# Kernel optimization log

Hardware: AMD Instinct MI355X
Metric: run time of the kernel (lower is better)

The kernel has to match this reference:

```python
import jax, jax.numpy as jnp
import numpy as np
from jax import lax

B, DIM, H, W = 8, 256, 48, 48
HEADS, DH = 8, 32
K, S = 5, 2
P = K // 2
SCALE = DH ** -0.5
EPS = 1e-5


def setup_inputs() -> dict:
    key = jax.random.key(0)
    ks = jax.random.split(key, 12)
    w = lambda k, sh: jax.random.normal(k, sh, jnp.float32) * 0.02
    return {
        'x': jax.random.normal(ks[0], (B, DIM, H, W), jnp.float32),
        'kv': jax.random.normal(ks[1], (B, DIM, H, W), jnp.float32),
        'wq': w(ks[2], (DIM, DIM)), 'bq': jnp.zeros((DIM,), jnp.float32),
        'wk': w(ks[3], (DIM, DIM)), 'bk': jnp.zeros((DIM,), jnp.float32),
        'wv': w(ks[4], (DIM, DIM)), 'bv': jnp.zeros((DIM,), jnp.float32),
        'w_dw': w(ks[5], (DH, 1, K, K)), 'b_dw': jnp.zeros((DH,), jnp.float32),
        'ln_w': jnp.ones((DH,), jnp.float32), 'ln_b': jnp.zeros((DH,), jnp.float32),
        'w_off': w(ks[6], (2, DH)),
        'wo': w(ks[7], (DIM, DIM)), 'bo': jnp.zeros((DIM,), jnp.float32),
    }


def conv1x1(x, w, b=None):
    # x: (B, Cin, H, W), w: (Cout, Cin)
    y = jnp.einsum('oc,bchw->bohw', w, x)
    return y if b is None else y + b[None, :, None, None]


def grid_sample_bilinear(inp, grid):
    # inp: (N, C, Hh, Ww); grid: (N, Hg, Wg, 2) in (x, y), align_corners=True
    N, C, Hh, Ww = inp.shape
    gx = (grid[..., 0] + 1.0) * 0.5 * (Ww - 1)
    gy = (grid[..., 1] + 1.0) * 0.5 * (Hh - 1)
    x0 = jnp.floor(gx)
    y0 = jnp.floor(gy)
    wx = gx - x0  # frac weights for x1/y1 corners
    wy = gy - y0
    x0i = jnp.clip(x0.astype(jnp.int32), 0, Ww - 1)
    x1i = jnp.clip(x0.astype(jnp.int32) + 1, 0, Ww - 1)
    y0i = jnp.clip(y0.astype(jnp.int32), 0, Hh - 1)
    y1i = jnp.clip(y0.astype(jnp.int32) + 1, 0, Hh - 1)
    flat = inp.reshape(N, C, Hh * Ww)
    n = grid.shape[1] * grid.shape[2]

    def gather(yi, xi):
        idx = (yi * Ww + xi).reshape(N, 1, n)
        return jnp.take_along_axis(flat, jnp.broadcast_to(idx, (N, C, n)), axis=2)

    w00 = ((1 - wx) * (1 - wy)).reshape(N, 1, n)
    w01 = (wx * (1 - wy)).reshape(N, 1, n)
    w10 = ((1 - wx) * wy).reshape(N, 1, n)
    w11 = (wx * wy).reshape(N, 1, n)
    return (w00 * gather(y0i, x0i) + w01 * gather(y0i, x1i)
            + w10 * gather(y1i, x0i) + w11 * gather(y1i, x1i))  # (N, C, n)


def reference(x, kv, wq, bq, wk, bk, wv, bv, w_dw, b_dw, ln_w, ln_b, w_off, wo, bo):
    q = conv1x1(x, wq, bq)                      # (B, DIM, H, W)
    q_off = q.reshape(B * HEADS, DH, H, W)      # per-head channels
    # depthwise offset conv
    t = lax.conv_general_dilated(q_off, w_dw, (S, S), [(P, P), (P, P)],
                                 feature_group_count=DH,
                                 dimension_numbers=('NCHW', 'OIHW', 'NCHW'))
    t = t + b_dw[None, :, None, None]
    Hk, Wk = t.shape[2], t.shape[3]
    n = Hk * Wk
    # LayerNormProxy: LN over channel dim
    t = t.transpose(0, 2, 3, 1)                 # (BH, Hk, Wk, DH)
    mu = t.mean(-1, keepdims=True)
    var = ((t - mu) ** 2).mean(-1, keepdims=True)
    t = (t - mu) / jnp.sqrt(var + EPS) * ln_w + ln_b
    t = jax.nn.gelu(t, approximate=False)
    offset = jnp.einsum('oc,bhwc->bhwo', w_off, t)  # (BH, Hk, Wk, 2) as (y, x)
    # reference points, normalized to [-1, 1]
    ref_y = (jnp.linspace(0.5, Hk - 0.5, Hk, dtype=jnp.float32) / (Hk - 1.0)) * 2.0 - 1.0
    ref_x = (jnp.linspace(0.5, Wk - 0.5, Wk, dtype=jnp.float32) / (Wk - 1.0)) * 2.0 - 1.0
    ref = jnp.stack(jnp.meshgrid(ref_y, ref_x, indexing='ij'), axis=-1)  # (Hk, Wk, 2)
    pos = jnp.clip(offset + ref[None], -1.0, 1.0)
    grid = pos[..., ::-1]                       # (x, y) order for sampling
    kvs = grid_sample_bilinear(kv.reshape(B * HEADS, DH, H, W), grid)  # (BH, DH, n)
    kv4 = kvs.reshape(B, DIM, 1, n)
    k = conv1x1(kv4, wk, bk).reshape(B * HEADS, DH, n)
    v = conv1x1(kv4, wv, bv).reshape(B * HEADS, DH, n)
    qf = q.reshape(B * HEADS, DH, H * W)
    attn = jax.nn.softmax(jnp.einsum('bcm,bcn->bmn', qf, k) * SCALE, axis=2)
    out = jnp.einsum('bmn,bcn->bcm', attn, v).reshape(B, DIM, H, W)
    return conv1x1(out, wo, bo)
```

## Files before the change

### kernel.cpp

```cpp
#include <hip/hip_runtime.h>
#include <hip/hip_bf16.h>
#include <cstddef>

#define BB 8
#define DIM 256
#define HH 48
#define WW 48
#define HW 2304
#define HEADS 8
#define DH 32
#define BH 64
#define HK 24
#define WK 24
#define NN 576
#define SCALE 0.17677669529663687f
#define EPSF 1e-5f

typedef __attribute__((ext_vector_type(8))) short short8;
typedef __attribute__((ext_vector_type(4))) float f32x4;

static __device__ inline short f2bf_s(float f) {
  __hip_bfloat16 h = __float2bfloat16(f);
  return *reinterpret_cast<short*>(&h);
}

static __device__ inline unsigned pkrnd(float a, float b) {
  unsigned ua = __builtin_bit_cast(unsigned, a) + 0x8000u;
  unsigned ub = __builtin_bit_cast(unsigned, b) + 0x8000u;
  return __builtin_amdgcn_perm(ub, ua, 0x07060302);
}

static __device__ inline void split8(const float* xf, short8& bh, short8& bl) {
  union { unsigned u[4]; short8 v; } H, L;
#pragma unroll
  for (int p = 0; p < 4; p++) {
    float x0 = xf[2 * p], x1 = xf[2 * p + 1];
    unsigned u0 = __builtin_bit_cast(unsigned, x0) & 0xffff0000u;
    unsigned u1 = __builtin_bit_cast(unsigned, x1) & 0xffff0000u;
    float l0 = x0 - __builtin_bit_cast(float, u0);
    float l1 = x1 - __builtin_bit_cast(float, u1);
    H.u[p] = __builtin_amdgcn_perm(u1, u0, 0x07060302);
    L.u[p] = __builtin_amdgcn_perm(__builtin_bit_cast(unsigned, l1),
                                   __builtin_bit_cast(unsigned, l0), 0x07060302);
  }
  bh = H.v;
  bl = L.v;
}

__global__ __launch_bounds__(256) void prep(
    const float* __restrict__ x,
    const float* __restrict__ wq, const float* __restrict__ wk,
    const float* __restrict__ wv, const float* __restrict__ wo,
    short* __restrict__ Xh, short* __restrict__ Xl,
    short* __restrict__ Wqh, short* __restrict__ Wql,
    short* __restrict__ Wkh, short* __restrict__ Wkl,
    short* __restrict__ Wvh, short* __restrict__ Wvl,
    short* __restrict__ Woh, short* __restrict__ Wol) {
  const int bid = blockIdx.x;
  if (bid < 1152) {
    __shared__ float t[64][65];
    int mt = bid % 36, t2 = bid / 36;
    int ct = t2 & 3, b = t2 >> 2;
    const int c0 = ct * 64, m0 = mt * 64;
    const int col = threadIdx.x & 63, row4 = threadIdx.x >> 6;
    const float* xb = x + ((size_t)b * 256 + c0) * HW + m0;
#pragma unroll
    for (int k = 0; k < 16; k++) {
      int c = row4 + k * 4;
      t[c][col] = xb[(size_t)c * HW + col];
    }
    __syncthreads();
    short* oh = Xh + ((size_t)b * HW + m0) * 256 + c0;
    short* ol = Xl + ((size_t)b * HW + m0) * 256 + c0;
#pragma unroll
    for (int k = 0; k < 16; k++) {
      int m = row4 + k * 4;
      float v = t[col][m];
      unsigned u = __builtin_bit_cast(unsigned, v) & 0xffff0000u;
      float rem = v - __builtin_bit_cast(float, u);
      oh[(size_t)m * 256 + col] = (short)(u >> 16);
      ol[(size_t)m * 256 + col] = (short)(__builtin_bit_cast(unsigned, rem) >> 16);
    }
  } else {
    const float* srcs[4] = {wq, wk, wv, wo};
    short* his[4] = {Wqh, Wkh, Wvh, Woh};
    short* los[4] = {Wql, Wkl, Wvl, Wol};
    int e0 = (bid - 1152) * 1024 + threadIdx.x * 4;
    int w = e0 >> 16, off = e0 & 65535;
    float4 v4 = *(const float4*)(srcs[w] + off);
    float vv[4] = {v4.x, v4.y, v4.z, v4.w};
    union { short s[4]; int2 i2; } Hu, Lu;
#pragma unroll
    for (int j = 0; j < 4; j++) {
      unsigned u = __builtin_bit_cast(unsigned, vv[j]) & 0xffff0000u;
      float rem = vv[j] - __builtin_bit_cast(float, u);
      Hu.s[j] = (short)(u >> 16);
      Lu.s[j] = (short)(__builtin_bit_cast(unsigned, rem) >> 16);
    }
    *(int2*)(his[w] + off) = Hu.i2;
    *(int2*)(los[w] + off) = Lu.i2;
  }
}

__global__ __launch_bounds__(256) void gemm_q_mfma(const short* __restrict__ Wh,
                                                   const short* __restrict__ Wl,
                                                   const float* __restrict__ bias,
                                                   const short* __restrict__ Xh,
                                                   const short* __restrict__ Xl,
                                                   float* __restrict__ Y) {
  const int tid = threadIdx.x;
  const int wave = tid >> 6;
  const int lane = tid & 63;
  const int quad = lane >> 4, l15 = lane & 15;
  const int b = blockIdx.y;
  const int oBase = wave * 64;
  const int mBase = blockIdx.x * 64;

  f32x4 acc[4][4] = {};
  for (int kc = 0; kc < 256; kc += 32) {
    short8 ah[4], al[4];
#pragma unroll
    for (int os = 0; os < 4; os++) {
      ah[os] = *(const short8*)(Wh + (size_t)(oBase + os * 16 + l15) * 256 + kc + quad * 8);
      al[os] = *(const short8*)(Wl + (size_t)(oBase + os * 16 + l15) * 256 + kc + quad * 8);
    }
#pragma unroll
    for (int mt = 0; mt < 4; mt++) {
      short8 bh_ = *(const short8*)(Xh + ((size_t)b * HW + mBase + mt * 16 + l15) * 256 + kc + quad * 8);
      short8 bl_ = *(const short8*)(Xl + ((size_t)b * HW + mBase + mt * 16 + l15) * 256 + kc + quad * 8);
#pragma unroll
      for (int os = 0; os < 4; os++) {
        acc[os][mt] = __builtin_amdgcn_mfma_f32_16x16x32_bf16(ah[os], bh_, acc[os][mt], 0, 0, 0);
        acc[os][mt] = __builtin_amdgcn_mfma_f32_16x16x32_bf16(al[os], bh_, acc[os][mt], 0, 0, 0);
        acc[os][mt] = __builtin_amdgcn_mfma_f32_16x16x32_bf16(ah[os], bl_, acc[os][mt], 0, 0, 0);
      }
    }
  }

#pragma unroll
  for (int os = 0; os < 4; os++)
#pragma unroll
    for (int r = 0; r < 4; r++) {
      int o = oBase + os * 16 + quad * 4 + r;
      float bs = bias[o];
      float* yp = Y + ((size_t)b * 256 + o) * HW + mBase + l15;
#pragma unroll
      for (int mt = 0; mt < 4; mt++) yp[mt * 16] = acc[os][mt][r] + bs;
    }
}

__global__ __launch_bounds__(64) void dw_sample_kernel(
    const float* __restrict__ q, const float* __restrict__ kv,
    const float* __restrict__ w_dw, const float* __restrict__ b_dw,
    const float* __restrict__ ln_w, const float* __restrict__ ln_b,
    const float* __restrict__ w_off, short* __restrict__ kvsTh,
    short* __restrict__ kvsTl) {
  __shared__ float s_wdw[DH * 25];
  __shared__ float s_bdw[DH], s_lnw[DH], s_lnb[DH], s_woff[2 * DH];
  const int tid = threadIdx.x;
  for (int i = tid; i < DH * 25; i += 64) s_wdw[i] = w_dw[i];
  if (tid < DH) { s_bdw[tid] = b_dw[tid]; s_lnw[tid] = ln_w[tid]; s_lnb[tid] = ln_b[tid]; }
  if (tid < 2 * DH) s_woff[tid] = w_off[tid];
  __syncthreads();

  const int nl = tid & 15, cg = tid >> 4;
  const int c0 = cg * 8;
  const int bh = blockIdx.x / (NN / 16);
  const int ntile = blockIdx.x - bh * (NN / 16);
  const int n = ntile * 16 + nl;
  const int yk = n / WK, xk = n - yk * WK;

  const float* qb = q + (size_t)bh * DH * HW;
  float t[8];
#pragma unroll
  for (int j = 0; j < 8; j++) t[j] = s_bdw[c0 + j];

  const int y0r = yk * 2 - 2, x0r = xk * 2 - 2;
  for (int dy = 0; dy < 5; dy++) {
    int y = y0r + dy;
    if (y < 0 || y >= HH) continue;
    for (int dx = 0; dx < 5; dx++) {
      int x = x0r + dx;
      if (x < 0 || x >= WW) continue;
      int off = y * WW + x;
      int widx = dy * 5 + dx;
#pragma unroll
      for (int j = 0; j < 8; j++)
        t[j] += s_wdw[(c0 + j) * 25 + widx] * qb[(size_t)(c0 + j) * HW + off];
    }
  }

  float mu = 0.f;
#pragma unroll
  for (int j = 0; j < 8; j++) mu += t[j];
  mu += __shfl_xor(mu, 16);
  mu += __shfl_xor(mu, 32);
  mu *= (1.0f / DH);
  float var = 0.f;
#pragma unroll
  for (int j = 0; j < 8; j++) { float d = t[j] - mu; var += d * d; }
  var += __shfl_xor(var, 16);
  var += __shfl_xor(var, 32);
  var *= (1.0f / DH);
  float rstd = rsqrtf(var + EPSF);

  float o0 = 0.f, o1 = 0.f;
#pragma unroll
  for (int j = 0; j < 8; j++) {
    float xn = (t[j] - mu) * rstd * s_lnw[c0 + j] + s_lnb[c0 + j];
    float g = 0.5f * xn * (1.0f + erff(xn * 0.70710678118654752f));
    o0 += s_woff[c0 + j] * g;
    o1 += s_woff[DH + c0 + j] * g;
  }
  o0 += __shfl_xor(o0, 16);
  o0 += __shfl_xor(o0, 32);
  o1 += __shfl_xor(o1, 16);
  o1 += __shfl_xor(o1, 32);

  const float ref_y = (0.5f + (float)yk) / 23.0f * 2.0f - 1.0f;
  const float ref_x = (0.5f + (float)xk) / 23.0f * 2.0f - 1.0f;
  float py = fminf(fmaxf(o0 + ref_y, -1.0f), 1.0f);
  float px = fminf(fmaxf(o1 + ref_x, -1.0f), 1.0f);

  float gx = (px + 1.0f) * 0.5f * 47.0f;
  float gy = (py + 1.0f) * 0.5f * 47.0f;
  float x0f = floorf(gx), y0f = floorf(gy);
  float wx = gx - x0f, wy = gy - y0f;
  int x0 = (int)x0f, y0 = (int)y0f;
  int x0i = min(max(x0, 0), WW - 1);
  int x1i = min(max(x0 + 1, 0), WW - 1);
  int y0i = min(max(y0, 0), HH - 1);
  int y1i = min(max(y0 + 1, 0), HH - 1);
  float w00 = (1.f - wx) * (1.f - wy);
  float w01 = wx * (1.f - wy);
  float w10 = (1.f - wx) * wy;
  float w11 = wx * wy;
  int i00 = y0i * WW + x0i, i01 = y0i * WW + x1i;
  int i10 = y1i * WW + x0i, i11 = y1i * WW + x1i;

  const float* kvb = kv + ((size_t)bh * DH + c0) * HW;
  float val[8];
#pragma unroll
  for (int j = 0; j < 8; j++) {
    const float* p = kvb + (size_t)j * HW;
    val[j] = w00 * p[i00] + w01 * p[i01] + w10 * p[i10] + w11 * p[i11];
  }
  short8 hv, lv;
  split8(val, hv, lv);
  size_t idx = ((size_t)(bh >> 3) * NN + n) * 256 + (bh & 7) * DH + c0;
  *(short8*)(kvsTh + idx) = hv;
  *(short8*)(kvsTl + idx) = lv;
}

__global__ __launch_bounds__(256) void kv_gemm_mfma(
    const short* __restrict__ Wkh, const short* __restrict__ Wkl,
    const float* __restrict__ bk,
    const short* __restrict__ Wvh, const short* __restrict__ Wvl,
    const float* __restrict__ bv,
    const short* __restrict__ Xh, const short* __restrict__ Xl,
    short* __restrict__ Kb, short* __restrict__ Vb) {
  const int tid = threadIdx.x;
  const int wave = tid >> 6;
  const int lane = tid & 63;
  const int quad = lane >> 4, l15 = lane & 15;
  const int b = blockIdx.z;
  const int mode = blockIdx.y >> 2;
  const int oTile = (blockIdx.y & 3) * 64;
  const int nBase = blockIdx.x * 64;

  if (mode == 0) {
    const int nW = nBase + wave * 16;
    const short* arh = Xh + ((size_t)b * NN + nW + l15) * 256 + quad * 8;
    const short* arl = Xl + ((size_t)b * NN + nW + l15) * 256 + quad * 8;
    f32x4 acc[4] = {};
    for (int kc = 0; kc < 256; kc += 32) {
      short8 ah = *(const short8*)(arh + kc);
      short8 al = *(const short8*)(arl + kc);
#pragma unroll
      for (int ot = 0; ot < 4; ot++) {
        short8 bh_ = *(const short8*)(Wkh + (size_t)(oTile + ot * 16 + l15) * 256 + kc + quad * 8);
        short8 bl_ = *(const short8*)(Wkl + (size_t)(oTile + ot * 16 + l15) * 256 + kc + quad * 8);
        acc[ot] = __builtin_amdgcn_mfma_f32_16x16x32_bf16(ah, bh_, acc[ot], 0, 0, 0);
        acc[ot] = __builtin_amdgcn_mfma_f32_16x16x32_bf16(al, bh_, acc[ot], 0, 0, 0);
        acc[ot] = __builtin_amdgcn_mfma_f32_16x16x32_bf16(ah, bl_, acc[ot], 0, 0, 0);
      }
    }
    float bs[4];
#pragma unroll
    for (int ot = 0; ot < 4; ot++) bs[ot] = bk[oTile + ot * 16 + l15];
#pragma unroll
    for (int r = 0; r < 4; r++) {
      short* yp = Kb + ((size_t)b * NN + nW + quad * 4 + r) * 256 + oTile + l15;
#pragma unroll
      for (int ot = 0; ot < 4; ot++) yp[ot * 16] = f2bf_s(acc[ot][r] + bs[ot]);
    }
  } else {
    const int oW = oTile + wave * 16;
    const short* arh = Wvh + (size_t)(oW + l15) * 256 + quad * 8;
    const short* arl = Wvl + (size_t)(oW + l15) * 256 + quad * 8;
    f32x4 acc[4] = {};
    for (int kc = 0; kc < 256; kc += 32) {
      short8 ah = *(const short8*)(arh + kc);
      short8 al = *(const short8*)(arl + kc);
#pragma unroll
      for (int nt = 0; nt < 4; nt++) {
        short8 bh_ = *(const short8*)(Xh + ((size_t)b * NN + nBase + nt * 16 + l15) * 256 + kc + quad * 8);
        short8 bl_ = *(const short8*)(Xl + ((size_t)b * NN + nBase + nt * 16 + l15) * 256 + kc + quad * 8);
        acc[nt] = __builtin_amdgcn_mfma_f32_16x16x32_bf16(ah, bh_, acc[nt], 0, 0, 0);
        acc[nt] = __builtin_amdgcn_mfma_f32_16x16x32_bf16(al, bh_, acc[nt], 0, 0, 0);
        acc[nt] = __builtin_amdgcn_mfma_f32_16x16x32_bf16(ah, bl_, acc[nt], 0, 0, 0);
      }
    }
#pragma unroll
    for (int r = 0; r < 4; r++) {
      int o = oW + quad * 4 + r;
      float bs = bv[o];
      short* yp = Vb + ((size_t)b * 256 + o) * NN + nBase + l15;
#pragma unroll
      for (int nt = 0; nt < 4; nt++) yp[nt * 16] = f2bf_s(acc[nt][r] + bs);
    }
  }
}

__global__ __launch_bounds__(256) void attn_mfma(const float* __restrict__ q,
                                                 const short* __restrict__ Kb,
                                                 const short* __restrict__ Vb,
                                                 short* __restrict__ O) {
  __shared__ short sK[2][64 * 40];
  __shared__ short sV[2][32 * 88];
  __shared__ int sP[4][2][256];
  const int tid = threadIdx.x;
  const int wave = tid >> 6;
  const int lane = tid & 63;
  const int quad = lane >> 4;
  const int l15 = lane & 15;
  const int bh = blockIdx.y;
  const int b = bh >> 3, head = bh & 7;
  const int mBase = blockIdx.x * 128 + wave * 32;

  short8 bq[2];
#pragma unroll
  for (int mt = 0; mt < 2; mt++) {
    const float* qp = q + ((size_t)bh * DH + quad * 8) * HW + mBase + mt * 16 + l15;
    short8 v;
#pragma unroll
    for (int j = 0; j < 8; j++) v[j] = f2bf_s(qp[(size_t)j * HW] * SCALE);
    bq[mt] = v;
  }

  const int kn = tid >> 2, kc = (tid & 3) * 8;
  const int vc = tid >> 3, vn = (tid & 7) * 8;
  const short* kg = Kb + (size_t)b * NN * 256 + head * DH;
  const short* vg = Vb + ((size_t)b * 256 + head * DH) * NN;

  short8 kreg = *(const short8*)(kg + (size_t)kn * 256 + kc);
  short8 vreg = *(const short8*)(vg + (size_t)vc * NN + vn);
  *(short8*)(&sK[0][kn * 40 + kc]) = kreg;
  *(short8*)(&sV[0][vc * 88 + vn]) = vreg;
  __syncthreads();

  const int g = (l15 >> 1) & 3;
  const int row16 = l15 * 16;
  const int wr0 = row16 + (((quad >> 1) ^ g) << 2) + ((quad & 1) << 1);
  const int wr1 = row16 + (((2 + (quad >> 1)) ^ g) << 2) + ((quad & 1) << 1);
  const int rd = row16 + ((quad ^ g) << 2);

  f32x4 oacc[2][2] = {};
  f32x4 dacc[2] = {};
  const short ONE = 0x3F80;
  const short8 ones = {ONE, ONE, ONE, ONE, ONE, ONE, ONE, ONE};

  for (int s = 0; s < 9; s++) {
    const int buf = s & 1;
    if (s + 1 < 9) {
      kreg = *(const short8*)(kg + (size_t)((s + 1) * 64 + kn) * 256 + kc);
      vreg = *(const short8*)(vg + (size_t)vc * NN + (s + 1) * 64 + vn);
    }
#pragma unroll
    for (int nt = 0; nt < 2; nt++) {
      short8 ka0 = *(const short8*)(&sK[buf][(nt * 32 + l15) * 40 + quad * 8]);
      short8 ka1 = *(const short8*)(&sK[buf][(nt * 32 + 16 + l15) * 40 + quad * 8]);
      short8 va0 = *(const short8*)(&sV[buf][l15 * 88 + nt * 32 + quad * 8]);
      short8 va1 = *(const short8*)(&sV[buf][(16 + l15) * 88 + nt * 32 + quad * 8]);
      f32x4 z = {0.f, 0.f, 0.f, 0.f};
      f32x4 st[2][2];
      st[0][0] = __builtin_amdgcn_mfma_f32_16x16x32_bf16(ka0, bq[0], z, 0, 0, 0);
      st[0][1] = __builtin_amdgcn_mfma_f32_16x16x32_bf16(ka1, bq[0], z, 0, 0, 0);
      st[1][0] = __builtin_amdgcn_mfma_f32_16x16x32_bf16(ka0, bq[1], z, 0, 0, 0);
      st[1][1] = __builtin_amdgcn_mfma_f32_16x16x32_bf16(ka1, bq[1], z, 0, 0, 0);
#pragma unroll
      for (int mt = 0; mt < 2; mt++) {
        float p0 = __expf(st[mt][0][0]), p1 = __expf(st[mt][0][1]);
        float p2 = __expf(st[mt][0][2]), p3 = __expf(st[mt][0][3]);
        float p4 = __expf(st[mt][1][0]), p5 = __expf(st[mt][1][1]);
        float p6 = __expf(st[mt][1][2]), p7 = __expf(st[mt][1][3]);
        int* base = &sP[wave][mt][0];
        *(int2*)(base + wr0) = make_int2((int)pkrnd(p0, p1), (int)pkrnd(p2, p3));
        *(int2*)(base + wr1) = make_int2((int)pkrnd(p4, p5), (int)pkrnd(p6, p7));
      }
#pragma unroll
      for (int mt = 0; mt < 2; mt++) {
        short8 pa = *(short8*)(&sP[wave][mt][0] + rd);
        oacc[mt][0] = __builtin_amdgcn_mfma_f32_16x16x32_bf16(pa, va0, oacc[mt][0], 0, 0, 0);
        oacc[mt][1] = __builtin_amdgcn_mfma_f32_16x16x32_bf16(pa, va1, oacc[mt][1], 0, 0, 0);
        dacc[mt] = __builtin_amdgcn_mfma_f32_16x16x32_bf16(pa, ones, dacc[mt], 0, 0, 0);
      }
    }
    if (s + 1 < 9) {
      *(short8*)(&sK[buf ^ 1][kn * 40 + kc]) = kreg;
      *(short8*)(&sV[buf ^ 1][vc * 88 + vn]) = vreg;
    }
    __syncthreads();
  }

#pragma unroll
  for (int mt = 0; mt < 2; mt++) {
    short* ob = O + ((size_t)b * HW + mBase + mt * 16) * 256 + head * DH + l15;
#pragma unroll
    for (int r = 0; r < 4; r++) {
      float inv = 1.0f / dacc[mt][r];
      ob[(size_t)(quad * 4 + r) * 256] = f2bf_s(oacc[mt][0][r] * inv);
      ob[(size_t)(quad * 4 + r) * 256 + 16] = f2bf_s(oacc[mt][1][r] * inv);
    }
  }
}

__global__ __launch_bounds__(256) void wo_gemm_mfma(const short* __restrict__ Whi,
                                                    const short* __restrict__ Wlo,
                                                    const float* __restrict__ bias,
                                                    const short* __restrict__ X,
                                                    float* __restrict__ Y) {
  const int tid = threadIdx.x;
  const int wave = tid >> 6;
  const int lane = tid & 63;
  const int quad = lane >> 4;
  const int l15 = lane & 15;
  const int b = blockIdx.y;
  const int oBase = wave * 64;
  const int mBase = blockIdx.x * 64;

  f32x4 acc[4][4] = {};
  for (int kc = 0; kc < 256; kc += 32) {
    short8 ah[4], al[4];
#pragma unroll
    for (int os = 0; os < 4; os++) {
      ah[os] = *(const short8*)(Whi + (size_t)(oBase + os * 16 + l15) * 256 + kc + quad * 8);
      al[os] = *(const short8*)(Wlo + (size_t)(oBase + os * 16 + l15) * 256 + kc + quad * 8);
    }
#pragma unroll
    for (int mt = 0; mt < 4; mt++) {
      short8 bx = *(const short8*)(X + ((size_t)b * HW + mBase + mt * 16 + l15) * 256 + kc + quad * 8);
#pragma unroll
      for (int os = 0; os < 4; os++) {
        acc[os][mt] = __builtin_amdgcn_mfma_f32_16x16x32_bf16(ah[os], bx, acc[os][mt], 0, 0, 0);
        acc[os][mt] = __builtin_amdgcn_mfma_f32_16x16x32_bf16(al[os], bx, acc[os][mt], 0, 0, 0);
      }
    }
  }

#pragma unroll
  for (int os = 0; os < 4; os++)
#pragma unroll
    for (int r = 0; r < 4; r++) {
      int o = oBase + os * 16 + quad * 4 + r;
      float bs = bias[o];
      float* yp = Y + ((size_t)b * 256 + o) * HW + mBase + l15;
#pragma unroll
      for (int mt = 0; mt < 4; mt++) yp[mt * 16] = acc[os][mt][r] + bs;
    }
}

extern "C" void kernel_launch(void* const* d_in, const int* in_sizes, int n_in,
                              void* d_out, int out_size, void* d_ws, size_t ws_size,
                              hipStream_t stream) {
  const float* x    = (const float*)d_in[0];
  const float* kv   = (const float*)d_in[1];
  const float* wq   = (const float*)d_in[2];
  const float* bq   = (const float*)d_in[3];
  const float* wk   = (const float*)d_in[4];
  const float* bk   = (const float*)d_in[5];
  const float* wv   = (const float*)d_in[6];
  const float* bv   = (const float*)d_in[7];
  const float* w_dw = (const float*)d_in[8];
  const float* b_dw = (const float*)d_in[9];
  const float* ln_w = (const float*)d_in[10];
  const float* ln_b = (const float*)d_in[11];
  const float* w_off= (const float*)d_in[12];
  const float* wo   = (const float*)d_in[13];
  const float* bo   = (const float*)d_in[14];
  float* out = (float*)d_out;
  float* ws = (float*)d_ws;

  float* q     = ws;
  short* Xth   = (short*)(ws + 4718592);
  short* O     = (short*)(ws + 4718592);
  short* Xtl   = (short*)(ws + 7077888);
  short* kvsTh = (short*)(ws + 7077888);
  short* kvsTl = (short*)(ws + 7667712);
  short* Kb    = (short*)(ws + 8257536);
  short* Vb    = (short*)(ws + 8847360);
  short* Wqh   = (short*)(ws + 9437184);
  short* Wql = Wqh + 65536;
  short* Wkh = Wql + 65536;
  short* Wkl = Wkh + 65536;
  short* Wvh = Wkl + 65536;
  short* Wvl = Wvh + 65536;
  short* Woh = Wvl + 65536;
  short* Wol = Woh + 65536;

  prep<<<dim3(1408), dim3(256), 0, stream>>>(x, wq, wk, wv, wo, Xth, Xtl,
                                             Wqh, Wql, Wkh, Wkl, Wvh, Wvl, Woh, Wol);
  gemm_q_mfma<<<dim3(HW / 64, BB), dim3(256), 0, stream>>>(Wqh, Wql, bq, Xth, Xtl, q);
  dw_sample_kernel<<<dim3(BH * NN / 16), dim3(64), 0, stream>>>(
      q, kv, w_dw, b_dw, ln_w, ln_b, w_off, kvsTh, kvsTl);
  kv_gemm_mfma<<<dim3(NN / 64, 8, BB), dim3(256), 0, stream>>>(
      Wkh, Wkl, bk, Wvh, Wvl, bv, kvsTh, kvsTl, Kb, Vb);
  attn_mfma<<<dim3(HW / 128, BH), dim3(256), 0, stream>>>(q, Kb, Vb, O);
  wo_gemm_mfma<<<dim3(HW / 64, BB), dim3(256), 0, stream>>>(Woh, Wol, bo, O, out);
}
```

Before: 264.4 us.

## Transpose kv to channel-last in prep and remap dw_sample to one thread per channel

Adds a transpose of kv into channel-last layout inside the prep kernel, staged in the output buffer as scratch. The depthwise-conv/offset/sample kernel now uses one thread per channel with 32 lanes per sample point, so the bilinear gathers and stores become coalesced across channels. Per-channel weights now sit in registers, and the reductions become full 32-lane shuffles. The cost is an extra full read and write of kv (about 19 MB each way) in prep, and the q loads in the conv are now strided across channels.

```diff
diff --git a/kernel.cpp b/kernel.cpp
--- a/kernel.cpp
+++ b/kernel.cpp
@@ -48,17 +48,18 @@
 }
 
 __global__ __launch_bounds__(256) void prep(
-    const float* __restrict__ x,
+    const float* __restrict__ x, const float* __restrict__ kv,
     const float* __restrict__ wq, const float* __restrict__ wk,
     const float* __restrict__ wv, const float* __restrict__ wo,
     short* __restrict__ Xh, short* __restrict__ Xl,
+    float* __restrict__ kvT,
     short* __restrict__ Wqh, short* __restrict__ Wql,
     short* __restrict__ Wkh, short* __restrict__ Wkl,
     short* __restrict__ Wvh, short* __restrict__ Wvl,
     short* __restrict__ Woh, short* __restrict__ Wol) {
+  __shared__ float t[64][65];
   const int bid = blockIdx.x;
   if (bid < 1152) {
-    __shared__ float t[64][65];
     int mt = bid % 36, t2 = bid / 36;
     int ct = t2 & 3, b = t2 >> 2;
     const int c0 = ct * 64, m0 = mt * 64;
@@ -81,11 +82,30 @@
       oh[(size_t)m * 256 + col] = (short)(u >> 16);
       ol[(size_t)m * 256 + col] = (short)(__builtin_bit_cast(unsigned, rem) >> 16);
     }
+  } else if (bid < 2304) {
+    int bb = bid - 1152;
+    int mt = bb % 36, t2 = bb / 36;
+    int ct = t2 & 3, b = t2 >> 2;
+    const int c0 = ct * 64, m0 = mt * 64;
+    const int col = threadIdx.x & 63, row4 = threadIdx.x >> 6;
+    const float* xb = kv + ((size_t)b * 256 + c0) * HW + m0;
+#pragma unroll
+    for (int k = 0; k < 16; k++) {
+      int c = row4 + k * 4;
+      t[c][col] = xb[(size_t)c * HW + col];
+    }
+    __syncthreads();
+    float* ot = kvT + ((size_t)b * HW + m0) * 256 + c0;
+#pragma unroll
+    for (int k = 0; k < 16; k++) {
+      int m = row4 + k * 4;
+      ot[(size_t)m * 256 + col] = t[col][m];
+    }
   } else {
     const float* srcs[4] = {wq, wk, wv, wo};
     short* his[4] = {Wqh, Wkh, Wvh, Woh};
     short* los[4] = {Wql, Wkl, Wvl, Wol};
-    int e0 = (bid - 1152) * 1024 + threadIdx.x * 4;
+    int e0 = (bid - 2304) * 1024 + threadIdx.x * 4;
     int w = e0 >> 16, off = e0 & 65535;
     float4 v4 = *(const float4*)(srcs[w] + off);
     float vv[4] = {v4.x, v4.y, v4.z, v4.w};
@@ -149,73 +169,67 @@
     }
 }
 
-__global__ __launch_bounds__(64) void dw_sample_kernel(
-    const float* __restrict__ q, const float* __restrict__ kv,
+__global__ __launch_bounds__(256) void dw_sample_kernel(
+    const float* __restrict__ q, const float* __restrict__ kvT,
     const float* __restrict__ w_dw, const float* __restrict__ b_dw,
     const float* __restrict__ ln_w, const float* __restrict__ ln_b,
     const float* __restrict__ w_off, short* __restrict__ kvsTh,
     short* __restrict__ kvsTl) {
-  __shared__ float s_wdw[DH * 25];
-  __shared__ float s_bdw[DH], s_lnw[DH], s_lnb[DH], s_woff[2 * DH];
   const int tid = threadIdx.x;
-  for (int i = tid; i < DH * 25; i += 64) s_wdw[i] = w_dw[i];
-  if (tid < DH) { s_bdw[tid] = b_dw[tid]; s_lnw[tid] = ln_w[tid]; s_lnb[tid] = ln_b[tid]; }
-  if (tid < 2 * DH) s_woff[tid] = w_off[tid];
-  __syncthreads();
-
-  const int nl = tid & 15, cg = tid >> 4;
-  const int c0 = cg * 8;
-  const int bh = blockIdx.x / (NN / 16);
-  const int ntile = blockIdx.x - bh * (NN / 16);
-  const int n = ntile * 16 + nl;
+  const int ch = tid & 31;
+  const int np = tid >> 5;
+  const int bid = blockIdx.x;
+  const int b = bid & 7;
+  const int r = bid >> 3;
+  const int head = r / 72;
+  const int ntile = r - head * 72;
+  const int bh = b * 8 + head;
+  const int n = ntile * 8 + np;
   const int yk = n / WK, xk = n - yk * WK;
 
-  const float* qb = q + (size_t)bh * DH * HW;
-  float t[8];
-#pragma unroll
-  for (int j = 0; j < 8; j++) t[j] = s_bdw[c0 + j];
-
+  float wreg[25];
+  {
+    const float* wp = w_dw + ch * 25;
+#pragma unroll
+    for (int i = 0; i < 25; i++) wreg[i] = wp[i];
+  }
+  float t = b_dw[ch];
+
+  const float* qb = q + (size_t)(bh * DH + ch) * HW;
   const int y0r = yk * 2 - 2, x0r = xk * 2 - 2;
+#pragma unroll
   for (int dy = 0; dy < 5; dy++) {
     int y = y0r + dy;
-    if (y < 0 || y >= HH) continue;
+    if ((unsigned)y >= HH) continue;
+    const float* qrow = qb + y * WW;
+#pragma unroll
     for (int dx = 0; dx < 5; dx++) {
       int x = x0r + dx;
-      if (x < 0 || x >= WW) continue;
-      int off = y * WW + x;
-      int widx = dy * 5 + dx;
-#pragma unroll
-      for (int j = 0; j < 8; j++)
-        t[j] += s_wdw[(c0 + j) * 25 + widx] * qb[(size_t)(c0 + j) * HW + off];
-    }
-  }
-
-  float mu = 0.f;
-#pragma unroll
-  for (int j = 0; j < 8; j++) mu += t[j];
-  mu += __shfl_xor(mu, 16);
-  mu += __shfl_xor(mu, 32);
+      if ((unsigned)x >= WW) continue;
+      t += wreg[dy * 5 + dx] * qrow[x];
+    }
+  }
+
+  float mu = t;
+#pragma unroll
+  for (int m = 1; m < 32; m <<= 1) mu += __shfl_xor(mu, m);
   mu *= (1.0f / DH);
-  float var = 0.f;
-#pragma unroll
-  for (int j = 0; j < 8; j++) { float d = t[j] - mu; var += d * d; }
-  var += __shfl_xor(var, 16);
-  var += __shfl_xor(var, 32);
+  float d = t - mu;
+  float var = d * d;
+#pragma unroll
+  for (int m = 1; m < 32; m <<= 1) var += __shfl_xor(var, m);
   var *= (1.0f / DH);
   float rstd = rsqrtf(var + EPSF);
 
-  float o0 = 0.f, o1 = 0.f;
-#pragma unroll
-  for (int j = 0; j < 8; j++) {
-    float xn = (t[j] - mu) * rstd * s_lnw[c0 + j] + s_lnb[c0 + j];
-    float g = 0.5f * xn * (1.0f + erff(xn * 0.70710678118654752f));
-    o0 += s_woff[c0 + j] * g;
-    o1 += s_woff[DH + c0 + j] * g;
-  }
-  o0 += __shfl_xor(o0, 16);
-  o0 += __shfl_xor(o0, 32);
-  o1 += __shfl_xor(o1, 16);
-  o1 += __shfl_xor(o1, 32);
+  float xn = d * rstd * ln_w[ch] + ln_b[ch];
+  float g = 0.5f * xn * (1.0f + erff(xn * 0.70710678118654752f));
+  float o0 = w_off[ch] * g;
+  float o1 = w_off[DH + ch] * g;
+#pragma unroll
+  for (int m = 1; m < 32; m <<= 1) {
+    o0 += __shfl_xor(o0, m);
+    o1 += __shfl_xor(o1, m);
+  }
 
   const float ref_y = (0.5f + (float)yk) / 23.0f * 2.0f - 1.0f;
   const float ref_x = (0.5f + (float)xk) / 23.0f * 2.0f - 1.0f;
@@ -235,21 +249,19 @@
   float w01 = wx * (1.f - wy);
   float w10 = (1.f - wx) * wy;
   float w11 = wx * wy;
-  int i00 = y0i * WW + x0i, i01 = y0i * WW + x1i;
-  int i10 = y1i * WW + x0i, i11 = y1i * WW + x1i;
-
-  const float* kvb = kv + ((size_t)bh * DH + c0) * HW;
-  float val[8];
-#pragma unroll
-  for (int j = 0; j < 8; j++) {
-    const float* p = kvb + (size_t)j * HW;
-    val[j] = w00 * p[i00] + w01 * p[i01] + w10 * p[i10] + w11 * p[i11];
-  }
-  short8 hv, lv;
-  split8(val, hv, lv);
-  size_t idx = ((size_t)(bh >> 3) * NN + n) * 256 + (bh & 7) * DH + c0;
-  *(short8*)(kvsTh + idx) = hv;
-  *(short8*)(kvsTl + idx) = lv;
+
+  const float* kvb = kvT + (size_t)b * HW * 256 + head * DH + ch;
+  float val = w00 * kvb[(size_t)(y0i * WW + x0i) * 256]
+            + w01 * kvb[(size_t)(y0i * WW + x1i) * 256]
+            + w10 * kvb[(size_t)(y1i * WW + x0i) * 256]
+            + w11 * kvb[(size_t)(y1i * WW + x1i) * 256];
+
+  unsigned ub = __builtin_bit_cast(unsigned, val);
+  unsigned uh = ub & 0xffff0000u;
+  float rem = val - __builtin_bit_cast(float, uh);
+  size_t idx = ((size_t)b * NN + n) * 256 + head * DH + ch;
+  kvsTh[idx] = (short)(uh >> 16);
+  kvsTl[idx] = (short)(__builtin_bit_cast(unsigned, rem) >> 16);
 }
 
 __global__ __launch_bounds__(256) void kv_gemm_mfma(
@@ -507,12 +519,13 @@
   short* Wvl = Wvh + 65536;
   short* Woh = Wvl + 65536;
   short* Wol = Woh + 65536;
-
-  prep<<<dim3(1408), dim3(256), 0, stream>>>(x, wq, wk, wv, wo, Xth, Xtl,
+  float* kvT = out;
+
+  prep<<<dim3(2560), dim3(256), 0, stream>>>(x, kv, wq, wk, wv, wo, Xth, Xtl, kvT,
                                              Wqh, Wql, Wkh, Wkl, Wvh, Wvl, Woh, Wol);
   gemm_q_mfma<<<dim3(HW / 64, BB), dim3(256), 0, stream>>>(Wqh, Wql, bq, Xth, Xtl, q);
-  dw_sample_kernel<<<dim3(BH * NN / 16), dim3(64), 0, stream>>>(
-      q, kv, w_dw, b_dw, ln_w, ln_b, w_off, kvsTh, kvsTl);
+  dw_sample_kernel<<<dim3(BH * NN / 8), dim3(256), 0, stream>>>(
+      q, kvT, w_dw, b_dw, ln_w, ln_b, w_off, kvsTh, kvsTl);
   kv_gemm_mfma<<<dim3(NN / 64, 8, BB), dim3(256), 0, stream>>>(
       Wkh, Wkl, bk, Wvh, Wvl, bv, kvsTh, kvsTl, Kb, Vb);
   attn_mfma<<<dim3(HW / 128, BH), dim3(256), 0, stream>>>(q, Kb, Vb, O);
```

After: 286.4 us. 1.08x slower.
